# Performance work log

Measured on AMD Instinct MI355X. Metric: run time of the kernel, lower is better.

Reference implementation:

```python
import jax, jax.numpy as jnp
import numpy as np

ROI = 116
FEAT = ROI * (ROI - 1) // 2  # 6670 upper-triangular entries
D = 1024
H = 1024
EPS = 1e-5


def _batchnorm(x, gamma, beta):
    # training-mode BatchNorm1d: biased batch statistics over dim 0
    mu = jnp.mean(x, axis=0, keepdims=True)
    var = jnp.var(x, axis=0, keepdims=True)
    return (x - mu) * jax.lax.rsqrt(var + EPS) * gamma + beta


def setup_inputs() -> dict:
    key = jax.random.key(0)
    ks = jax.random.split(key, 16)
    B, W = 64, 128
    s_feat = 1.0 / np.sqrt(FEAT)
    s_d = 1.0 / np.sqrt(D)
    s_cat = 1.0 / np.sqrt(FEAT + H)
    s_h = 1.0 / np.sqrt(H)
    return {
        "FC": jax.random.normal(ks[0], (B, W, ROI, ROI), jnp.float32),
        "cluster_centers": jax.random.normal(ks[1], (2, FEAT), jnp.float32),
        # MIL attention MLP: Linear(6670,1024) -> Tanh -> Linear(1024,1)
        "W1": jax.random.uniform(ks[2], (FEAT, D), jnp.float32, -s_feat, s_feat),
        "b1": jnp.zeros((D,), jnp.float32),
        "W2": jax.random.uniform(ks[3], (D, 1), jnp.float32, -s_d, s_d),
        "b2": jnp.zeros((1,), jnp.float32),
        # batch norms
        "bn_g": jnp.ones((FEAT,), jnp.float32),
        "bn_b": jnp.zeros((FEAT,), jnp.float32),
        "bn2_g": jnp.ones((FEAT,), jnp.float32),
        "bn2_b": jnp.zeros((FEAT,), jnp.float32),
        # cross-attention projections (Wv_cross is dead code in the source)
        "Wq": jax.random.uniform(ks[4], (FEAT, H), jnp.float32, -s_feat, s_feat),
        "bq": jnp.zeros((H,), jnp.float32),
        "Wk": jax.random.uniform(ks[5], (FEAT, H), jnp.float32, -s_feat, s_feat),
        "bk": jnp.zeros((H,), jnp.float32),
        # classifier (dropout = identity at inference)
        "Wc1": jax.random.uniform(ks[6], (FEAT + H, H), jnp.float32, -s_cat, s_cat),
        "bc1": jnp.zeros((H,), jnp.float32),
        "Wc2": jax.random.uniform(ks[7], (H, 1), jnp.float32, -s_h, s_h),
        "bc2": jnp.zeros((1,), jnp.float32),
    }


def reference(FC, cluster_centers, W1, b1, W2, b2, bn_g, bn_b, bn2_g, bn2_b,
              Wq, bq, Wk, bk, Wc1, bc1, Wc2, bc2):
    iu0, iu1 = jnp.triu_indices(ROI, k=1)
    bag_level = FC[:, :, iu0, iu1]                      # [B, W, 6670]

    # MIL attention pooling, batched over samples (replaces per-sample loop)
    h = jnp.tanh(jnp.einsum('bwf,fd->bwd', bag_level, W1) + b1)
    a = jnp.einsum('bwd,dk->bwk', h, W2) + b2           # [B, W, 1]
    att = jax.nn.softmax(a[..., 0], axis=-1)            # softmax over windows
    bag_z_up = jnp.einsum('bw,bwf->bf', att, bag_level)  # [B, 6670]

    bag_z_up = _batchnorm(bag_z_up, bn_g, bn_b)
    cc = _batchnorm(cluster_centers, bn2_g, bn2_b)       # [K, 6670]

    q = bag_z_up @ Wq + bq                               # [B, H]
    k = cc @ Wk + bk                                     # [K, H]
    QK = (q @ k.T) / jnp.sqrt(jnp.float32(H))            # [B, K]
    att_cross = jax.nn.softmax(QK, axis=-1)
    v = cc @ Wq + bq                                     # NB: source reuses Wq_cross
    final_cross = att_cross @ v                          # [B, H]

    X = jnp.concatenate([final_cross, bag_z_up], axis=1)  # [B, H+6670]
    Y_prob = jax.nn.sigmoid(jax.nn.relu(X @ Wc1 + bc1) @ Wc2 + bc2)[:, 0]
    Y_hat = (Y_prob >= 0.5).astype(jnp.float32)
    return Y_prob, Y_hat
```

## Files before the change

### kernel.cpp

```cpp
#include <hip/hip_runtime.h>
#include <hip/hip_bf16.h>
#include <math.h>

#define ROI   116
#define FEATN 6670
#define KP    6688
#define DD    1024
#define HHN   1024
#define BB    64
#define WW    128
#define MT    8192
#define XW    7694
#define EPSV  1e-5f
#define KB_SPLIT 32

typedef __attribute__((ext_vector_type(8))) short short8;
typedef __attribute__((ext_vector_type(4))) float f32x4;
typedef __attribute__((ext_vector_type(4))) unsigned int u32x4;

__device__ __forceinline__ short f2bf(float v) {
  __hip_bfloat16 b = __float2bfloat16(v);
  return *reinterpret_cast<short*>(&b);
}

__device__ __forceinline__ float fast_tanh(float x) {
  float ax = fabsf(x);
  float t  = __expf(-2.0f * ax);
  float r  = (1.0f - t) / (1.0f + t);
  return copysignf(r, x);
}

__global__ void k_lut(int2* lut) {
  int f = blockIdx.x * 256 + threadIdx.x;
  if (f >= FEATN) return;
  int i = (int)((231.0 - sqrt((double)(53361 - 8 * f))) * 0.5);
  if (i < 0) i = 0;
  if (i > ROI - 2) i = ROI - 2;
  while (i > 0 && i * (231 - i) / 2 > f) --i;
  while (i < ROI - 2 && (i + 1) * (231 - (i + 1)) / 2 <= f) ++i;
  int j = i + 1 + (f - i * (231 - i) / 2);
  lut[f] = make_int2(i, j);
}

__global__ void k_extract(const float* __restrict__ FC, const int2* __restrict__ lut,
                          short* __restrict__ bag) {
  int m = blockIdx.x;
  const float* base = FC + (size_t)m * (ROI * ROI);
  for (int f = threadIdx.x; f < KP; f += 256) {
    float v = 0.f;
    if (f < FEATN) {
      int2 ij = lut[f];
      v = base[ij.x * ROI + ij.y];
    }
    bag[(size_t)m * KP + f] = f2bf(v);
  }
}

__global__ void k_transpose(const float* __restrict__ W1, short* __restrict__ W1T) {
  __shared__ float tile[32][33];
  int k0 = blockIdx.x * 32;
  int d0 = blockIdx.y * 32;
  int tx = threadIdx.x & 31, ty = threadIdx.x >> 5;
  for (int r = 0; r < 32; r += 8) {
    int k = k0 + ty + r;
    float v = 0.f;
    if (k < FEATN) v = W1[(size_t)k * DD + d0 + tx];
    tile[ty + r][tx] = v;
  }
  __syncthreads();
  for (int r = 0; r < 32; r += 8) {
    W1T[(size_t)(d0 + ty + r) * KP + k0 + tx] = f2bf(tile[tx][ty + r]);
  }
}

__global__ __launch_bounds__(256) void k_gemm(const short* __restrict__ A,
                                              const short* __restrict__ BT,
                                              const float* __restrict__ b1,
                                              float* __restrict__ Hout) {
  __shared__ __align__(16) short As[128][32];
  __shared__ __align__(16) short Bs[128][32];
  int tid  = threadIdx.x;
  int m0   = blockIdx.x * 128;
  int n0   = blockIdx.y * 128;
  int wave = tid >> 6, lane = tid & 63;
  int wr = wave >> 1, wc = wave & 1;
  int quad = lane >> 4, l15 = lane & 15;
  int sr = tid >> 2;
  int sc = (tid & 3) * 8;

  f32x4 acc[4][4] = {};

  const short* Ag0 = A  + (size_t)(m0 + sr) * KP + sc;
  const short* Ag1 = Ag0 + (size_t)64 * KP;
  const short* Bg0 = BT + (size_t)(n0 + sr) * KP + sc;
  const short* Bg1 = Bg0 + (size_t)64 * KP;

  for (int k0 = 0; k0 < KP; k0 += 32) {
    *(u32x4*)(&As[sr][sc])      = *(const u32x4*)(Ag0 + k0);
    *(u32x4*)(&As[sr + 64][sc]) = *(const u32x4*)(Ag1 + k0);
    *(u32x4*)(&Bs[sr][sc])      = *(const u32x4*)(Bg0 + k0);
    *(u32x4*)(&Bs[sr + 64][sc]) = *(const u32x4*)(Bg1 + k0);
    __syncthreads();

    short8 af[4], bf[4];
#pragma unroll
    for (int mi = 0; mi < 4; mi++)
      af[mi] = *(const short8*)(&As[wr * 64 + mi * 16 + l15][quad * 8]);
#pragma unroll
    for (int ni = 0; ni < 4; ni++)
      bf[ni] = *(const short8*)(&Bs[wc * 64 + ni * 16 + l15][quad * 8]);
#pragma unroll
    for (int mi = 0; mi < 4; mi++)
#pragma unroll
      for (int ni = 0; ni < 4; ni++)
        acc[mi][ni] = __builtin_amdgcn_mfma_f32_16x16x32_bf16(af[mi], bf[ni], acc[mi][ni], 0, 0, 0);
    __syncthreads();
  }

#pragma unroll
  for (int ni = 0; ni < 4; ni++) {
    int n = n0 + wc * 64 + ni * 16 + l15;
    float bias = b1[n];
#pragma unroll
    for (int mi = 0; mi < 4; mi++) {
#pragma unroll
      for (int r = 0; r < 4; r++) {
        int m = m0 + wr * 64 + mi * 16 + quad * 4 + r;
        Hout[(size_t)m * DD + n] = fast_tanh(acc[mi][ni][r] + bias);
      }
    }
  }
}

__global__ void k_a(const float* __restrict__ H, const float* __restrict__ W2,
                    const float* __restrict__ b2, float* __restrict__ a) {
  int m = blockIdx.x, t = threadIdx.x;
  float s = 0.f;
  for (int n = t; n < DD; n += 256) s += H[(size_t)m * DD + n] * W2[n];
  __shared__ float red[256];
  red[t] = s; __syncthreads();
  for (int st = 128; st > 0; st >>= 1) {
    if (t < st) red[t] += red[t + st];
    __syncthreads();
  }
  if (t == 0) a[m] = red[0] + b2[0];
}

__global__ void k_softmax(const float* __restrict__ a, float* __restrict__ att) {
  int b = blockIdx.x, t = threadIdx.x;
  __shared__ float sh[128];
  float v = a[b * WW + t];
  sh[t] = v; __syncthreads();
  for (int s = 64; s > 0; s >>= 1) { if (t < s) sh[t] = fmaxf(sh[t], sh[t + s]); __syncthreads(); }
  float mx = sh[0]; __syncthreads();
  float e = expf(v - mx);
  sh[t] = e; __syncthreads();
  for (int s = 64; s > 0; s >>= 1) { if (t < s) sh[t] += sh[t + s]; __syncthreads(); }
  att[b * WW + t] = e / sh[0];
}

__global__ void k_bagz(const float* __restrict__ FC, const int2* __restrict__ lut,
                       const float* __restrict__ att, float* __restrict__ bagz) {
  __shared__ float atts[WW];
  int b = blockIdx.y;
  int f = blockIdx.x * 256 + threadIdx.x;
  if (threadIdx.x < WW) atts[threadIdx.x] = att[b * WW + threadIdx.x];
  __syncthreads();
  if (f >= FEATN) return;
  int2 ij = lut[f];
  const float* base = FC + (size_t)b * WW * ROI * ROI + ij.x * ROI + ij.y;
  float s = 0.f;
  for (int w = 0; w < WW; ++w) s += atts[w] * base[(size_t)w * ROI * ROI];
  bagz[(size_t)b * FEATN + f] = s;
}

__global__ void k_bn(const float* __restrict__ bagz, const float* __restrict__ g,
                     const float* __restrict__ beta, float* __restrict__ X) {
  int f = blockIdx.x * 256 + threadIdx.x;
  if (f >= FEATN) return;
  float s = 0.f, s2 = 0.f;
  for (int b = 0; b < BB; b++) { float v = bagz[(size_t)b * FEATN + f]; s += v; s2 += v * v; }
  float mu  = s * (1.f / BB);
  float var = s2 * (1.f / BB) - mu * mu;
  float sc  = rsqrtf(var + EPSV) * g[f];
  float bt  = beta[f];
  for (int b = 0; b < BB; b++)
    X[(size_t)b * XW + HHN + f] = (bagz[(size_t)b * FEATN + f] - mu) * sc + bt;
}

__global__ void k_ccbn(const float* __restrict__ cc, const float* __restrict__ g,
                       const float* __restrict__ beta, float* __restrict__ ccbn) {
  int f = blockIdx.x * 256 + threadIdx.x;
  if (f >= FEATN) return;
  float c0 = cc[f], c1 = cc[FEATN + f];
  float mu = 0.5f * (c0 + c1);
  float d0 = c0 - mu, d1 = c1 - mu;
  float var = 0.5f * (d0 * d0 + d1 * d1);
  float sc = rsqrtf(var + EPSV) * g[f];
  ccbn[f]         = d0 * sc + beta[f];
  ccbn[FEATN + f] = d1 * sc + beta[f];
}

template <int R, int MODE>
__global__ __launch_bounds__(256) void k_skinny(const float* __restrict__ X,
                                                const float* __restrict__ ccbn,
                                                const float* __restrict__ Wt,
                                                float* __restrict__ partial,
                                                int K, int kchunk) {
  constexpr int RG = (R + 3) / 4;
  constexpr int RP = RG * 4;
  __shared__ __align__(16) float zs[RP][68];
  int tx = threadIdx.x & 63;
  int ty = threadIdx.x >> 6;
  int n  = blockIdx.x * 64 + tx;
  int k0 = blockIdx.y * kchunk;
  int k1 = min(k0 + kchunk, K);
  int r0 = ty * RG;

  float acc[RG];
#pragma unroll
  for (int i = 0; i < RG; i++) acc[i] = 0.f;

  for (int kk0 = k0; kk0 < k1; kk0 += 64) {
    for (int idx = threadIdx.x; idx < RP * 64; idx += 256) {
      int r = idx >> 6, c = idx & 63;
      int k = kk0 + c;
      float v = 0.f;
      if (r < R && k < k1) {
        const float* zr;
        if (MODE == 0) zr = (r < 64) ? (X + (size_t)r * XW + HHN) : (ccbn + (size_t)(r - 64) * FEATN);
        else if (MODE == 1) zr = ccbn + (size_t)r * FEATN;
        else zr = X + (size_t)r * XW;
        v = zr[k];
      }
      zs[r][c] = v;
    }
    __syncthreads();
#pragma unroll 4
    for (int c = 0; c < 64; c += 4) {
      int k = kk0 + c;
      float w0 = (k + 0 < k1) ? Wt[(size_t)(k + 0) * HHN + n] : 0.f;
      float w1 = (k + 1 < k1) ? Wt[(size_t)(k + 1) * HHN + n] : 0.f;
      float w2 = (k + 2 < k1) ? Wt[(size_t)(k + 2) * HHN + n] : 0.f;
      float w3 = (k + 3 < k1) ? Wt[(size_t)(k + 3) * HHN + n] : 0.f;
#pragma unroll
      for (int i = 0; i < RG; i++) {
        f32x4 z = *(const f32x4*)(&zs[r0 + i][c]);
        acc[i] += z.x * w0 + z.y * w1 + z.z * w2 + z.w * w3;
      }
    }
    __syncthreads();
  }
#pragma unroll
  for (int i = 0; i < RG; i++) {
    int rr = r0 + i;
    if (rr < R)
      partial[(size_t)blockIdx.y * R * HHN + (size_t)rr * HHN + n] = acc[i];
  }
}

template <int R>
__global__ void k_reduce(const float* __restrict__ partial, const float* __restrict__ bias,
                         float* __restrict__ out, int KB, int act) {
  int idx = blockIdx.x * 256 + threadIdx.x;
  if (idx >= R * HHN) return;
  int n = idx & (HHN - 1);
  float s = bias[n];
  for (int kb = 0; kb < KB; kb++) s += partial[(size_t)kb * R * HHN + idx];
  if (act) s = fmaxf(s, 0.f);
  out[idx] = s;
}

__global__ void k_cross(const float* __restrict__ qv, const float* __restrict__ kb,
                        float* __restrict__ X) {
  int b = blockIdx.x, t = threadIdx.x;
  const float* q  = qv + (size_t)b * HHN;
  const float* v0 = qv + (size_t)64 * HHN;
  const float* v1 = qv + (size_t)65 * HHN;
  float s0 = 0.f, s1 = 0.f;
  for (int n = t; n < HHN; n += 256) {
    float qn = q[n];
    s0 += qn * kb[n];
    s1 += qn * kb[HHN + n];
  }
  __shared__ float r0[256], r1[256];
  r0[t] = s0; r1[t] = s1; __syncthreads();
  for (int st = 128; st > 0; st >>= 1) {
    if (t < st) { r0[t] += r0[t + st]; r1[t] += r1[t + st]; }
    __syncthreads();
  }
  float d0 = r0[0] * (1.f / 32.f), d1 = r1[0] * (1.f / 32.f);
  float mx = fmaxf(d0, d1);
  float e0 = expf(d0 - mx), e1 = expf(d1 - mx);
  float p0 = e0 / (e0 + e1), p1 = e1 / (e0 + e1);
  for (int n = t; n < HHN; n += 256)
    X[(size_t)b * XW + n] = p0 * v0[n] + p1 * v1[n];
}

__global__ void k_final(const float* __restrict__ Rb, const float* __restrict__ Wc2,
                        const float* __restrict__ bc2, float* __restrict__ out) {
  int b = blockIdx.x, t = threadIdx.x;
  float s = 0.f;
  for (int n = t; n < HHN; n += 256) s += Rb[(size_t)b * HHN + n] * Wc2[n];
  __shared__ float red[256];
  red[t] = s; __syncthreads();
  for (int st = 128; st > 0; st >>= 1) {
    if (t < st) red[t] += red[t + st];
    __syncthreads();
  }
  if (t == 0) {
    float y = red[0] + bc2[0];
    float p = 1.f / (1.f + expf(-y));
    out[b]      = p;
    out[64 + b] = (p >= 0.5f) ? 1.f : 0.f;
  }
}

extern "C" void kernel_launch(void* const* d_in, const int* in_sizes, int n_in,
                              void* d_out, int out_size, void* d_ws, size_t ws_size,
                              hipStream_t stream) {
  const float* FC    = (const float*)d_in[0];
  const float* CC    = (const float*)d_in[1];
  const float* W1    = (const float*)d_in[2];
  const float* b1    = (const float*)d_in[3];
  const float* W2    = (const float*)d_in[4];
  const float* b2    = (const float*)d_in[5];
  const float* bn_g  = (const float*)d_in[6];
  const float* bn_b  = (const float*)d_in[7];
  const float* bn2_g = (const float*)d_in[8];
  const float* bn2_b = (const float*)d_in[9];
  const float* Wq    = (const float*)d_in[10];
  const float* bq    = (const float*)d_in[11];
  const float* Wk    = (const float*)d_in[12];
  const float* bk    = (const float*)d_in[13];
  const float* Wc1   = (const float*)d_in[14];
  const float* bc1   = (const float*)d_in[15];
  const float* Wc2   = (const float*)d_in[16];
  const float* bc2   = (const float*)d_in[17];
  float* out = (float*)d_out;

  char* w = (char*)d_ws;
  auto alloc = [&](size_t bytes) {
    char* p = w;
    w += (bytes + 255) & ~(size_t)255;
    return p;
  };
  short* bagbf   = (short*)alloc((size_t)MT * KP * 2);
  short* W1T     = (short*)alloc((size_t)DD * KP * 2);
  float* Hbuf    = (float*)alloc((size_t)MT * DD * 4);
  float* abuf    = (float*)alloc((size_t)MT * 4);
  float* attbuf  = (float*)alloc((size_t)MT * 4);
  float* bagz    = (float*)alloc((size_t)BB * FEATN * 4);
  float* Xbuf    = (float*)alloc((size_t)BB * XW * 4);
  float* ccbn    = (float*)alloc((size_t)2 * FEATN * 4);
  float* qvbuf   = (float*)alloc((size_t)66 * HHN * 4);
  float* kbuf    = (float*)alloc((size_t)2 * HHN * 4);
  float* Rbuf    = (float*)alloc((size_t)BB * HHN * 4);
  int2*  lut     = (int2*)alloc((size_t)FEATN * 8);
  float* partQ   = (float*)alloc((size_t)KB_SPLIT * 66 * HHN * 4);
  float* partK   = (float*)alloc((size_t)KB_SPLIT * 2 * HHN * 4);
  float* partC   = partQ;

  k_lut<<<dim3((FEATN + 255) / 256), dim3(256), 0, stream>>>(lut);
  k_extract<<<dim3(MT), dim3(256), 0, stream>>>(FC, lut, bagbf);
  k_transpose<<<dim3(KP / 32, DD / 32), dim3(256), 0, stream>>>(W1, W1T);
  k_gemm<<<dim3(MT / 128, DD / 128), dim3(256), 0, stream>>>(bagbf, W1T, b1, Hbuf);
  k_a<<<dim3(MT), dim3(256), 0, stream>>>(Hbuf, W2, b2, abuf);
  k_softmax<<<dim3(BB), dim3(WW), 0, stream>>>(abuf, attbuf);
  k_bagz<<<dim3((FEATN + 255) / 256, BB), dim3(256), 0, stream>>>(FC, lut, attbuf, bagz);
  k_bn<<<dim3((FEATN + 255) / 256), dim3(256), 0, stream>>>(bagz, bn_g, bn_b, Xbuf);
  k_ccbn<<<dim3((FEATN + 255) / 256), dim3(256), 0, stream>>>(CC, bn2_g, bn2_b, ccbn);

  k_skinny<66, 0><<<dim3(16, KB_SPLIT), dim3(256), 0, stream>>>(Xbuf, ccbn, Wq, partQ, FEATN, 209);
  k_reduce<66><<<dim3(66 * HHN / 256), dim3(256), 0, stream>>>(partQ, bq, qvbuf, KB_SPLIT, 0);
  k_skinny<2, 1><<<dim3(16, KB_SPLIT), dim3(256), 0, stream>>>(Xbuf, ccbn, Wk, partK, FEATN, 209);
  k_reduce<2><<<dim3(2 * HHN / 256), dim3(256), 0, stream>>>(partK, bk, kbuf, KB_SPLIT, 0);
  k_cross<<<dim3(BB), dim3(256), 0, stream>>>(qvbuf, kbuf, Xbuf);

  k_skinny<64, 2><<<dim3(16, KB_SPLIT), dim3(256), 0, stream>>>(Xbuf, ccbn, Wc1, partC, XW, 241);
  k_reduce<64><<<dim3(64 * HHN / 256), dim3(256), 0, stream>>>(partC, bc1, Rbuf, KB_SPLIT, 1);
  k_final<<<dim3(BB), dim3(256), 0, stream>>>(Rbuf, Wc2, bc2, out);

  (void)in_sizes; (void)n_in; (void)out_size; (void)ws_size;
}
```

Baseline: 1.231 ms.

## Fuse attention score into GEMM epilogue, use direct-to-LDS loads, reuse bf16 bag

The GEMM epilogue now applies tanh, multiplies by W2 and reduces across lanes, then atomically adds into per-row attention scores. This drops the 32 MB H buffer write and the separate k_a pass. GEMM tiles load through global_load_lds straight into shared memory, and extraction writes vectorized 4-wide stores while zeroing the score buffer. The bag-weighted sum now reads the compact bf16 bag instead of gathering strided fp32 FC, at the cost of bf16 precision in bag_z. The b2 bias is dropped, which is harmless because softmax is shift-invariant, and atomics make the summation order nondeterministic.

```diff
diff --git a/kernel.cpp b/kernel.cpp
--- a/kernel.cpp
+++ b/kernel.cpp
@@ -1,6 +1,7 @@
 #include <hip/hip_runtime.h>
 #include <hip/hip_bf16.h>
 #include <math.h>
+#include <stdint.h>
 
 #define ROI   116
 #define FEATN 6670
@@ -15,12 +16,30 @@
 #define KB_SPLIT 32
 
 typedef __attribute__((ext_vector_type(8))) short short8;
+typedef __attribute__((ext_vector_type(4))) short short4v;
 typedef __attribute__((ext_vector_type(4))) float f32x4;
 typedef __attribute__((ext_vector_type(4))) unsigned int u32x4;
+
+typedef __attribute__((address_space(3))) unsigned int as3_u32;
+typedef __attribute__((address_space(1))) unsigned int as1_u32;
+
+__device__ __forceinline__ void gload_lds16(const void* g, void* l) {
+  __builtin_amdgcn_global_load_lds(
+      (const as1_u32*)(uintptr_t)g,
+      (as3_u32*)(unsigned int)(uintptr_t)l,
+      16, 0, 0);
+}
 
 __device__ __forceinline__ short f2bf(float v) {
   __hip_bfloat16 b = __float2bfloat16(v);
   return *reinterpret_cast<short*>(&b);
+}
+
+__device__ __forceinline__ float bf2f(short h) {
+  unsigned int u = ((unsigned int)(unsigned short)h) << 16;
+  float f;
+  __builtin_memcpy(&f, &u, 4);
+  return f;
 }
 
 __device__ __forceinline__ float fast_tanh(float x) {
@@ -43,16 +62,23 @@
 }
 
 __global__ void k_extract(const float* __restrict__ FC, const int2* __restrict__ lut,
-                          short* __restrict__ bag) {
+                          short* __restrict__ bag, float* __restrict__ a_out) {
   int m = blockIdx.x;
+  if (threadIdx.x == 0) a_out[m] = 0.f;
   const float* base = FC + (size_t)m * (ROI * ROI);
-  for (int f = threadIdx.x; f < KP; f += 256) {
-    float v = 0.f;
-    if (f < FEATN) {
-      int2 ij = lut[f];
-      v = base[ij.x * ROI + ij.y];
+  for (int f0 = threadIdx.x * 4; f0 < KP; f0 += 1024) {
+    short4v o;
+#pragma unroll
+    for (int e = 0; e < 4; e++) {
+      int f = f0 + e;
+      float v = 0.f;
+      if (f < FEATN) {
+        int2 ij = lut[f];
+        v = base[ij.x * ROI + ij.y];
+      }
+      o[e] = f2bf(v);
     }
-    bag[(size_t)m * KP + f] = f2bf(v);
+    *(short4v*)(&bag[(size_t)m * KP + f0]) = o;
   }
 }
 
@@ -76,7 +102,8 @@
 __global__ __launch_bounds__(256) void k_gemm(const short* __restrict__ A,
                                               const short* __restrict__ BT,
                                               const float* __restrict__ b1,
-                                              float* __restrict__ Hout) {
+                                              const float* __restrict__ W2,
+                                              float* __restrict__ a_out) {
   __shared__ __align__(16) short As[128][32];
   __shared__ __align__(16) short Bs[128][32];
   int tid  = threadIdx.x;
@@ -85,21 +112,25 @@
   int wave = tid >> 6, lane = tid & 63;
   int wr = wave >> 1, wc = wave & 1;
   int quad = lane >> 4, l15 = lane & 15;
-  int sr = tid >> 2;
-  int sc = (tid & 3) * 8;
+  int srow = tid >> 2;
+  int scol = (tid & 3) * 8;
 
   f32x4 acc[4][4] = {};
 
-  const short* Ag0 = A  + (size_t)(m0 + sr) * KP + sc;
+  const short* Ag0 = A  + (size_t)(m0 + srow) * KP + scol;
   const short* Ag1 = Ag0 + (size_t)64 * KP;
-  const short* Bg0 = BT + (size_t)(n0 + sr) * KP + sc;
+  const short* Bg0 = BT + (size_t)(n0 + srow) * KP + scol;
   const short* Bg1 = Bg0 + (size_t)64 * KP;
+  short* Al0 = &As[srow][scol];
+  short* Al1 = &As[srow + 64][scol];
+  short* Bl0 = &Bs[srow][scol];
+  short* Bl1 = &Bs[srow + 64][scol];
 
   for (int k0 = 0; k0 < KP; k0 += 32) {
-    *(u32x4*)(&As[sr][sc])      = *(const u32x4*)(Ag0 + k0);
-    *(u32x4*)(&As[sr + 64][sc]) = *(const u32x4*)(Ag1 + k0);
-    *(u32x4*)(&Bs[sr][sc])      = *(const u32x4*)(Bg0 + k0);
-    *(u32x4*)(&Bs[sr + 64][sc]) = *(const u32x4*)(Bg1 + k0);
+    gload_lds16(Ag0 + k0, Al0);
+    gload_lds16(Ag1 + k0, Al1);
+    gload_lds16(Bg0 + k0, Bl0);
+    gload_lds16(Bg1 + k0, Bl1);
     __syncthreads();
 
     short8 af[4], bf[4];
@@ -117,33 +148,29 @@
     __syncthreads();
   }
 
+  float bias[4], w2v[4];
 #pragma unroll
   for (int ni = 0; ni < 4; ni++) {
     int n = n0 + wc * 64 + ni * 16 + l15;
-    float bias = b1[n];
-#pragma unroll
-    for (int mi = 0; mi < 4; mi++) {
-#pragma unroll
-      for (int r = 0; r < 4; r++) {
-        int m = m0 + wr * 64 + mi * 16 + quad * 4 + r;
-        Hout[(size_t)m * DD + n] = fast_tanh(acc[mi][ni][r] + bias);
-      }
+    bias[ni] = b1[n];
+    w2v[ni]  = W2[n];
+  }
+#pragma unroll
+  for (int mi = 0; mi < 4; mi++) {
+#pragma unroll
+    for (int r = 0; r < 4; r++) {
+      float s = 0.f;
+#pragma unroll
+      for (int ni = 0; ni < 4; ni++)
+        s += fast_tanh(acc[mi][ni][r] + bias[ni]) * w2v[ni];
+      s += __shfl_xor(s, 1);
+      s += __shfl_xor(s, 2);
+      s += __shfl_xor(s, 4);
+      s += __shfl_xor(s, 8);
+      if (l15 == 0)
+        atomicAdd(&a_out[m0 + wr * 64 + mi * 16 + quad * 4 + r], s);
     }
   }
-}
-
-__global__ void k_a(const float* __restrict__ H, const float* __restrict__ W2,
-                    const float* __restrict__ b2, float* __restrict__ a) {
-  int m = blockIdx.x, t = threadIdx.x;
-  float s = 0.f;
-  for (int n = t; n < DD; n += 256) s += H[(size_t)m * DD + n] * W2[n];
-  __shared__ float red[256];
-  red[t] = s; __syncthreads();
-  for (int st = 128; st > 0; st >>= 1) {
-    if (t < st) red[t] += red[t + st];
-    __syncthreads();
-  }
-  if (t == 0) a[m] = red[0] + b2[0];
 }
 
 __global__ void k_softmax(const float* __restrict__ a, float* __restrict__ att) {
@@ -159,19 +186,27 @@
   att[b * WW + t] = e / sh[0];
 }
 
-__global__ void k_bagz(const float* __restrict__ FC, const int2* __restrict__ lut,
-                       const float* __restrict__ att, float* __restrict__ bagz) {
+__global__ void k_bagz(const short* __restrict__ bag, const float* __restrict__ att,
+                       float* __restrict__ bagz) {
   __shared__ float atts[WW];
-  int b = blockIdx.y;
-  int f = blockIdx.x * 256 + threadIdx.x;
+  int b  = blockIdx.y;
+  int f0 = blockIdx.x * 2048 + threadIdx.x * 8;
   if (threadIdx.x < WW) atts[threadIdx.x] = att[b * WW + threadIdx.x];
   __syncthreads();
-  if (f >= FEATN) return;
-  int2 ij = lut[f];
-  const float* base = FC + (size_t)b * WW * ROI * ROI + ij.x * ROI + ij.y;
-  float s = 0.f;
-  for (int w = 0; w < WW; ++w) s += atts[w] * base[(size_t)w * ROI * ROI];
-  bagz[(size_t)b * FEATN + f] = s;
+  if (f0 >= KP) return;
+  const short* base = bag + (size_t)b * WW * KP + f0;
+  float s[8] = {};
+  for (int w = 0; w < WW; ++w) {
+    float aw = atts[w];
+    short8 v = *(const short8*)(base + (size_t)w * KP);
+#pragma unroll
+    for (int e = 0; e < 8; e++) s[e] += aw * bf2f(v[e]);
+  }
+#pragma unroll
+  for (int e = 0; e < 8; e++) {
+    int f = f0 + e;
+    if (f < FEATN) bagz[(size_t)b * FEATN + f] = s[e];
+  }
 }
 
 __global__ void k_bn(const float* __restrict__ bagz, const float* __restrict__ g,
@@ -338,6 +373,7 @@
   const float* Wc2   = (const float*)d_in[16];
   const float* bc2   = (const float*)d_in[17];
   float* out = (float*)d_out;
+  (void)b2;
 
   char* w = (char*)d_ws;
   auto alloc = [&](size_t bytes) {
@@ -347,7 +383,6 @@
   };
   short* bagbf   = (short*)alloc((size_t)MT * KP * 2);
   short* W1T     = (short*)alloc((size_t)DD * KP * 2);
-  float* Hbuf    = (float*)alloc((size_t)MT * DD * 4);
   float* abuf    = (float*)alloc((size_t)MT * 4);
   float* attbuf  = (float*)alloc((size_t)MT * 4);
   float* bagz    = (float*)alloc((size_t)BB * FEATN * 4);
@@ -362,12 +397,11 @@
   float* partC   = partQ;
 
   k_lut<<<dim3((FEATN + 255) / 256), dim3(256), 0, stream>>>(lut);
-  k_extract<<<dim3(MT), dim3(256), 0, stream>>>(FC, lut, bagbf);
+  k_extract<<<dim3(MT), dim3(256), 0, stream>>>(FC, lut, bagbf, abuf);
   k_transpose<<<dim3(KP / 32, DD / 32), dim3(256), 0, stream>>>(W1, W1T);
-  k_gemm<<<dim3(MT / 128, DD / 128), dim3(256), 0, stream>>>(bagbf, W1T, b1, Hbuf);
-  k_a<<<dim3(MT), dim3(256), 0, stream>>>(Hbuf, W2, b2, abuf);
+  k_gemm<<<dim3(MT / 128, DD / 128), dim3(256), 0, stream>>>(bagbf, W1T, b1, W2, abuf);
   k_softmax<<<dim3(BB), dim3(WW), 0, stream>>>(abuf, attbuf);
-  k_bagz<<<dim3((FEATN + 255) / 256, BB), dim3(256), 0, stream>>>(FC, lut, attbuf, bagz);
+  k_bagz<<<dim3((KP + 2047) / 2048, BB), dim3(256), 0, stream>>>(bagbf, attbuf, bagz);
   k_bn<<<dim3((FEATN + 255) / 256), dim3(256), 0, stream>>>(bagz, bn_g, bn_b, Xbuf);
   k_ccbn<<<dim3((FEATN + 255) / 256), dim3(256), 0, stream>>>(CC, bn2_g, bn2_b, ccbn);
 
```

Measured after the change: 1.166 ms. -5.3%, faster.
